# Performance work log

Hardware: AMD Instinct MI355X
Metric: run time of the kernel (lower is better)

Reference implementation:

```python
import jax, jax.numpy as jnp
import numpy as np

N = 50000      # nodes
E = 600000     # edges (avg degree 12)
D = 128        # input_dim == hidden_dim (required: same Linear reused across pool layers)
OUT = 64       # output_dim
NUM_POOL = 2   # num_pool_layers


def setup_inputs() -> dict:
    key = jax.random.key(0)
    ks = jax.random.split(key, 8)
    s = 1.0 / np.sqrt(D)  # fan-in style scaling keeps repeated scatter-adds stable
    x = jax.random.normal(ks[0], (N, D), dtype=jnp.float32)
    edge_index = jax.random.randint(ks[1], (2, E), 0, N, dtype=jnp.int64)
    W1 = jax.random.normal(ks[2], (D, D), dtype=jnp.float32) * s
    b1 = jnp.zeros((D,), dtype=jnp.float32)
    W2 = jax.random.normal(ks[3], (D, D), dtype=jnp.float32) * s
    b2 = jnp.zeros((D,), dtype=jnp.float32)
    Wout = jax.random.normal(ks[4], (D, OUT), dtype=jnp.float32) * s
    bout = jnp.zeros((OUT,), dtype=jnp.float32)
    return {"x": x, "edge_index": edge_index, "W1": W1, "b1": b1,
            "W2": W2, "b2": b2, "Wout": Wout, "bout": bout}


def _gauss_seidel_pool(x, W, b, src, dst, num_layers):
    # PyG MessagePassing(aggr='add'): out[i] = sum_{edges (j->i)} lin(x[j]).
    # Nodes with no incoming edges become zero (propagate replaces x entirely).
    for _ in range(num_layers):
        m = x @ W + b                      # [N, out] linear once per node (== lin(x_j) per edge)
        x = jax.ops.segment_sum(m[src], dst, num_segments=N)  # gather + scatter-add
    return x


def reference(x, edge_index, W1, b1, W2, b2, Wout, bout):
    src = edge_index[0]  # x_j source
    dst = edge_index[1]  # aggregation target i
    h = _gauss_seidel_pool(x, W1, b1, src, dst, NUM_POOL)
    h = jax.nn.relu(h)                     # dropout = identity (eval mode)
    h = _gauss_seidel_pool(h, W2, b2, src, dst, NUM_POOL)
    h = jax.nn.relu(h)
    return h @ Wout + bout                 # [N, OUT]
```

## Files before the change

### kernel.cpp

```cpp
#include <hip/hip_runtime.h>


static inline int ceil_div(int a, int b) { return (a + b - 1) / b; }

typedef __attribute__((ext_vector_type(8))) short bf16x8;
typedef __attribute__((ext_vector_type(4))) float f32x4;

__device__ inline unsigned short f2bf(float f) {
    unsigned u = __float_as_uint(f);
    return (unsigned short)((u + 0x7fffu + ((u >> 16) & 1u)) >> 16);
}


__device__ void wprep_dev(const float* __restrict__ W, unsigned short* __restrict__ hi,
                          int total, int C, int g0, int G) {
    for (int t = g0; t < total; t += G) {
        int j = t & 7;
        int lane = (t >> 3) & 63;
        int f = t >> 9;
        int c = f & 3, ct = f >> 2;
        int k = c * 32 + (lane >> 4) * 8 + j;
        int col = ct * 16 + (lane & 15);
        hi[t] = f2bf(W[(size_t)k * C + col]);
    }
}

__global__ __launch_bounds__(256) void prep_kernel(const float* __restrict__ W1,
                                                   const float* __restrict__ W2,
                                                   const float* __restrict__ Wout,
                                                   unsigned short* __restrict__ W1hi,
                                                   unsigned short* __restrict__ W2hi,
                                                   unsigned short* __restrict__ Wohi,
                                                   int* __restrict__ cursor,
                                                   unsigned* __restrict__ stat,
                                                   int N, int nChunks) {
    int g0 = blockIdx.x * 256 + threadIdx.x;
    int G = gridDim.x * 256;
    for (int i = g0; i < N; i += G) cursor[i] = 0;
    for (int i = g0; i < nChunks; i += G) stat[i] = 0;
    wprep_dev(W1, W1hi, 128 * 128, 128, g0, G);
    wprep_dev(W2, W2hi, 128 * 128, 128, g0, G);
    wprep_dev(Wout, Wohi, 128 * 64, 64, g0, G);
}


__global__ __launch_bounds__(256) void hist_kernel(const int* __restrict__ dst,
                                                   int* __restrict__ deg, int E) {
    int e = blockIdx.x * 256 + threadIdx.x;
    if (e < E) atomicAdd(&deg[dst[e]], 1);
}

__global__ __launch_bounds__(256) void scan_fuse_kernel(const int* __restrict__ deg,
                                                        int* __restrict__ rp,
                                                        int* __restrict__ cursor,
                                                        unsigned* __restrict__ stat,
                                                        int N) {
    __shared__ int s[256];
    int c = blockIdx.x, tid = threadIdx.x;
    int i = c * 256 + tid;
    int v = (i < N) ? deg[i] : 0;
    s[tid] = v;
    __syncthreads();
    for (int off = 1; off < 256; off <<= 1) {
        int t = (tid >= off) ? s[tid - off] : 0;
        __syncthreads();
        s[tid] += t;
        __syncthreads();
    }
    int loc = s[tid] - v;
    int tot = s[255];
    __syncthreads();
    if (tid == 0) atomicExch(&stat[c], (unsigned)tot | 0x80000000u);

    unsigned mine = 0;
    if (tid < c) {
        unsigned u;
        do { u = atomicAdd(&stat[tid], 0u); } while (!(u & 0x80000000u));
        mine = u & 0x7fffffffu;
    }
    s[tid] = (int)mine;
    __syncthreads();
    for (int off = 128; off >= 1; off >>= 1) {
        if (tid < off) s[tid] += s[tid + off];
        __syncthreads();
    }
    int prefix = s[0];
    if (i <= N) {
        int val = loc + prefix;
        rp[i] = val;
        if (i < N) cursor[i] = val;
    }
}

__global__ __launch_bounds__(256) void fill_kernel(const int* __restrict__ src,
                                                   const int* __restrict__ dst,
                                                   int* __restrict__ cursor,
                                                   unsigned short* __restrict__ es, int E) {
    int e = blockIdx.x * 256 + threadIdx.x;
    if (e < E) {
        int p = atomicAdd(&cursor[dst[e]], 1);
        es[p] = (unsigned short)src[e];
    }
}


__global__ __launch_bounds__(256) void gemm1_kernel(const float* __restrict__ X,
                                                    const uint4* __restrict__ Whi,
                                                    const float* __restrict__ Bias,
                                                    unsigned short* __restrict__ Y, int n) {
    int tid = threadIdx.x;
    int wave = tid >> 6, lane = tid & 63;
    int lm = lane & 15, lq = lane >> 4;
    int r0 = blockIdx.x * 64;

    bf16x8 afr[4][4];
#pragma unroll
    for (int rt = 0; rt < 4; ++rt) {
        int ar = r0 + rt * 16 + lm;
        if (ar > n - 1) ar = n - 1;
#pragma unroll
        for (int c = 0; c < 4; ++c) {
            int k = c * 32 + lq * 8;
            const float* ap = X + (size_t)ar * 128 + k;
            float4 f0 = ((const float4*)ap)[0];
            float4 f1 = ((const float4*)ap)[1];
            bf16x8 v;
            v[0] = (short)f2bf(f0.x); v[1] = (short)f2bf(f0.y);
            v[2] = (short)f2bf(f0.z); v[3] = (short)f2bf(f0.w);
            v[4] = (short)f2bf(f1.x); v[5] = (short)f2bf(f1.y);
            v[6] = (short)f2bf(f1.z); v[7] = (short)f2bf(f1.w);
            afr[rt][c] = v;
        }
    }

    f32x4 acc[4][2];
#pragma unroll
    for (int rt = 0; rt < 4; ++rt)
#pragma unroll
        for (int t = 0; t < 2; ++t)
            acc[rt][t] = (f32x4){0.f, 0.f, 0.f, 0.f};

#pragma unroll
    for (int c = 0; c < 4; ++c) {
#pragma unroll
        for (int t = 0; t < 2; ++t) {
            int ct = wave * 2 + t;
            uint4 uh = Whi[(ct * 4 + c) * 64 + lane];
            bf16x8 wh = *(const bf16x8*)&uh;
#pragma unroll
            for (int rt = 0; rt < 4; ++rt)
                acc[rt][t] = __builtin_amdgcn_mfma_f32_16x16x32_bf16(afr[rt][c], wh, acc[rt][t], 0, 0, 0);
        }
    }

#pragma unroll
    for (int t = 0; t < 2; ++t) {
        int col = (wave * 2 + t) * 16 + lm;
        float bias = Bias[col];
#pragma unroll
        for (int rt = 0; rt < 4; ++rt) {
#pragma unroll
            for (int r = 0; r < 4; ++r) {
                int row = r0 + rt * 16 + lq * 4 + r;
                if (row < n)
                    Y[(size_t)row * 128 + col] = f2bf(acc[rt][t][r] + bias);
            }
        }
    }
}


__device__ inline void acc_row8(float* a, uint4 v) {
    a[0] += __uint_as_float(v.x << 16);
    a[1] += __uint_as_float(v.x & 0xffff0000u);
    a[2] += __uint_as_float(v.y << 16);
    a[3] += __uint_as_float(v.y & 0xffff0000u);
    a[4] += __uint_as_float(v.z << 16);
    a[5] += __uint_as_float(v.z & 0xffff0000u);
    a[6] += __uint_as_float(v.w << 16);
    a[7] += __uint_as_float(v.w & 0xffff0000u);
}

template <int COLS, bool OUTF32>
__global__ __launch_bounds__(256) void fused_agg_gemm_kernel(const unsigned short* __restrict__ M,
                                                             const int* __restrict__ rp,
                                                             const unsigned short* __restrict__ es,
                                                             const uint4* __restrict__ Whi,
                                                             const float* __restrict__ Bias,
                                                             void* __restrict__ Yv,
                                                             int n, int do_relu) {
    constexpr int CT_W = COLS / 64;
    constexpr int SR = 136;
    __shared__ unsigned short Hl[64 * SR];
    __shared__ int rpl[65];
    __shared__ unsigned char perm[64];

    int tid = threadIdx.x;
    int r0 = blockIdx.x * 64;

    if (tid < 65) {
        int gi = r0 + tid;
        if (gi > n) gi = n;
        rpl[tid] = rp[gi];
    }
    __syncthreads();

    if (tid < 64) {
        int di = rpl[tid + 1] - rpl[tid];
        int rank = 0;
        for (int j = 0; j < 64; ++j) {
            int dj = rpl[j + 1] - rpl[j];
            rank += (dj > di) || (dj == di && j < tid);
        }
        perm[rank] = (unsigned char)tid;
    }
    __syncthreads();

    {
        int g = tid >> 4, ln = tid & 15;
#pragma unroll 1
        for (int q = 0; q < 4; ++q) {
            int nl = perm[q * 16 + g];
            int beg = rpl[nl], end = rpl[nl + 1];
            float acc[8] = {};
            int e = beg;
            for (; e + 8 <= end; e += 8) {
                int s0 = es[e],     s1 = es[e + 1], s2 = es[e + 2], s3 = es[e + 3];
                int s4 = es[e + 4], s5 = es[e + 5], s6 = es[e + 6], s7 = es[e + 7];
                uint4 v0 = ((const uint4*)(M + (size_t)s0 * 128))[ln];
                uint4 v1 = ((const uint4*)(M + (size_t)s1 * 128))[ln];
                uint4 v2 = ((const uint4*)(M + (size_t)s2 * 128))[ln];
                uint4 v3 = ((const uint4*)(M + (size_t)s3 * 128))[ln];
                uint4 v4 = ((const uint4*)(M + (size_t)s4 * 128))[ln];
                uint4 v5 = ((const uint4*)(M + (size_t)s5 * 128))[ln];
                uint4 v6 = ((const uint4*)(M + (size_t)s6 * 128))[ln];
                uint4 v7 = ((const uint4*)(M + (size_t)s7 * 128))[ln];
                acc_row8(acc, v0); acc_row8(acc, v1);
                acc_row8(acc, v2); acc_row8(acc, v3);
                acc_row8(acc, v4); acc_row8(acc, v5);
                acc_row8(acc, v6); acc_row8(acc, v7);
            }
            for (; e + 4 <= end; e += 4) {
                int s0 = es[e], s1 = es[e + 1], s2 = es[e + 2], s3 = es[e + 3];
                uint4 v0 = ((const uint4*)(M + (size_t)s0 * 128))[ln];
                uint4 v1 = ((const uint4*)(M + (size_t)s1 * 128))[ln];
                uint4 v2 = ((const uint4*)(M + (size_t)s2 * 128))[ln];
                uint4 v3 = ((const uint4*)(M + (size_t)s3 * 128))[ln];
                acc_row8(acc, v0); acc_row8(acc, v1);
                acc_row8(acc, v2); acc_row8(acc, v3);
            }
            for (; e < end; ++e) {
                uint4 v = ((const uint4*)(M + (size_t)es[e] * 128))[ln];
                acc_row8(acc, v);
            }
            if (do_relu) {
#pragma unroll
                for (int i = 0; i < 8; ++i) acc[i] = fmaxf(acc[i], 0.f);
            }
            uint4 o;
            o.x = (unsigned)f2bf(acc[0]) | ((unsigned)f2bf(acc[1]) << 16);
            o.y = (unsigned)f2bf(acc[2]) | ((unsigned)f2bf(acc[3]) << 16);
            o.z = (unsigned)f2bf(acc[4]) | ((unsigned)f2bf(acc[5]) << 16);
            o.w = (unsigned)f2bf(acc[6]) | ((unsigned)f2bf(acc[7]) << 16);
            *(uint4*)(&Hl[nl * SR + ln * 8]) = o;
        }
    }
    __syncthreads();

    int wave = tid >> 6, lane = tid & 63;
    int lm = lane & 15, lq = lane >> 4;

    f32x4 acc[4][CT_W];
#pragma unroll
    for (int rt = 0; rt < 4; ++rt)
#pragma unroll
        for (int t = 0; t < CT_W; ++t)
            acc[rt][t] = (f32x4){0.f, 0.f, 0.f, 0.f};

#pragma unroll
    for (int c = 0; c < 4; ++c) {
        bf16x8 afr[4];
#pragma unroll
        for (int rt = 0; rt < 4; ++rt)
            afr[rt] = *(const bf16x8*)(&Hl[(rt * 16 + lm) * SR + c * 32 + lq * 8]);
#pragma unroll
        for (int t = 0; t < CT_W; ++t) {
            int ct = wave * CT_W + t;
            uint4 uh = Whi[(ct * 4 + c) * 64 + lane];
            bf16x8 wh = *(const bf16x8*)&uh;
#pragma unroll
            for (int rt = 0; rt < 4; ++rt)
                acc[rt][t] = __builtin_amdgcn_mfma_f32_16x16x32_bf16(afr[rt], wh, acc[rt][t], 0, 0, 0);
        }
    }

#pragma unroll
    for (int t = 0; t < CT_W; ++t) {
        int col = (wave * CT_W + t) * 16 + lm;
        float bias = Bias[col];
#pragma unroll
        for (int rt = 0; rt < 4; ++rt) {
#pragma unroll
            for (int r = 0; r < 4; ++r) {
                int row = r0 + rt * 16 + lq * 4 + r;
                if (row < n) {
                    float v = acc[rt][t][r] + bias;
                    if (OUTF32)
                        ((float*)Yv)[(size_t)row * COLS + col] = v;
                    else
                        ((unsigned short*)Yv)[(size_t)row * COLS + col] = f2bf(v);
                }
            }
        }
    }
}


extern "C" void kernel_launch(void* const* d_in, const int* in_sizes, int n_in,
                              void* d_out, int out_size, void* d_ws, size_t ws_size,
                              hipStream_t stream) {
    const float* x    = (const float*)d_in[0];
    const int*   ei   = (const int*)d_in[1];
    const float* W1   = (const float*)d_in[2];
    const float* b1   = (const float*)d_in[3];
    const float* W2   = (const float*)d_in[4];
    const float* b2   = (const float*)d_in[5];
    const float* Wout = (const float*)d_in[6];
    const float* bout = (const float*)d_in[7];
    float*       out  = (float*)d_out;

    const int N = in_sizes[0] / 128;
    const int E = in_sizes[1] / 2;
    const int* src = ei;
    const int* dst = ei + E;

    char* ws = (char*)d_ws;
    auto take = [&](size_t bytes) {
        char* p = ws;
        ws += (bytes + 255) & ~(size_t)255;
        return p;
    };
    unsigned short* mA = (unsigned short*)take((size_t)N * 128 * 2);
    unsigned short* mB = (unsigned short*)take((size_t)N * 128 * 2);
    unsigned short* W1hi = (unsigned short*)take(128 * 128 * 2);
    unsigned short* W2hi = (unsigned short*)take(128 * 128 * 2);
    unsigned short* Wohi = (unsigned short*)take(128 * 64 * 2);
    int* rp      = (int*)take((size_t)(N + 1) * sizeof(int));
    int* cursor  = (int*)take((size_t)N * sizeof(int));
    unsigned short* es = (unsigned short*)take((size_t)E * sizeof(unsigned short));
    unsigned* stat = (unsigned*)take(4096);

    const int nChunks = ceil_div(N + 1, 256);
    const int tiles64 = ceil_div(N, 64);

    prep_kernel<<<256, 256, 0, stream>>>(W1, W2, Wout, W1hi, W2hi, Wohi,
                                         cursor, stat, N, nChunks);
    hist_kernel<<<ceil_div(E, 256), 256, 0, stream>>>(dst, cursor, E);
    scan_fuse_kernel<<<nChunks, 256, 0, stream>>>(cursor, rp, cursor, stat, N);
    fill_kernel<<<ceil_div(E, 256), 256, 0, stream>>>(src, dst, cursor, es, E);
    gemm1_kernel<<<tiles64, 256, 0, stream>>>(x, (const uint4*)W1hi, b1, mA, N);

    fused_agg_gemm_kernel<128, false><<<tiles64, 256, 0, stream>>>(
        mA, rp, es, (const uint4*)W1hi, b1, mB, N, 0);
    fused_agg_gemm_kernel<128, false><<<tiles64, 256, 0, stream>>>(
        mB, rp, es, (const uint4*)W2hi, b2, mA, N, 1);
    fused_agg_gemm_kernel<128, false><<<tiles64, 256, 0, stream>>>(
        mA, rp, es, (const uint4*)W2hi, b2, mB, N, 0);
    fused_agg_gemm_kernel<64, true><<<tiles64, 256, 0, stream>>>(
        mB, rp, es, (const uint4*)Wohi, bout, out, N, 1);
}
```

Before: 288.1 us.

## Reorder to aggregate-then-transform with degree-scaled bias and fused output GEMM

Uses linearity (sum of x_j W + b equals (sum x_j) W + deg*b) to aggregate raw features before each GEMM, removing the standalone first GEMM kernel in favour of a bf16 conversion of x in the prep kernel. The final GEMM with Wout is fused into the last aggregation kernel through shared memory, dropping one full-size kernel and its intermediate round trip. The gather loop now processes two destination nodes per thread group for more memory-level parallelism. It adds an extra bf16 copy of x and changes rounding order, so numerics differ slightly.

After: 337.3 us. 17.1% more time.

```diff
diff --git a/kernel.cpp b/kernel.cpp
--- a/kernel.cpp
+++ b/kernel.cpp
@@ -25,9 +25,11 @@
     }
 }
 
-__global__ __launch_bounds__(256) void prep_kernel(const float* __restrict__ W1,
+__global__ __launch_bounds__(256) void prep_kernel(const float* __restrict__ x,
+                                                   const float* __restrict__ W1,
                                                    const float* __restrict__ W2,
                                                    const float* __restrict__ Wout,
+                                                   unsigned short* __restrict__ xb,
                                                    unsigned short* __restrict__ W1hi,
                                                    unsigned short* __restrict__ W2hi,
                                                    unsigned short* __restrict__ Wohi,
@@ -38,6 +40,15 @@
     int G = gridDim.x * 256;
     for (int i = g0; i < N; i += G) cursor[i] = 0;
     for (int i = g0; i < nChunks; i += G) stat[i] = 0;
+
+    int nq = N * 32;
+    for (int i = g0; i < nq; i += G) {
+        float4 v = ((const float4*)x)[i];
+        ushort4 o;
+        o.x = f2bf(v.x); o.y = f2bf(v.y); o.z = f2bf(v.z); o.w = f2bf(v.w);
+        ((ushort4*)xb)[i] = o;
+    }
+
     wprep_dev(W1, W1hi, 128 * 128, 128, g0, G);
     wprep_dev(W2, W2hi, 128 * 128, 128, g0, G);
     wprep_dev(Wout, Wohi, 128 * 64, 64, g0, G);
@@ -104,72 +115,6 @@
 }
 
 
-__global__ __launch_bounds__(256) void gemm1_kernel(const float* __restrict__ X,
-                                                    const uint4* __restrict__ Whi,
-                                                    const float* __restrict__ Bias,
-                                                    unsigned short* __restrict__ Y, int n) {
-    int tid = threadIdx.x;
-    int wave = tid >> 6, lane = tid & 63;
-    int lm = lane & 15, lq = lane >> 4;
-    int r0 = blockIdx.x * 64;
-
-    bf16x8 afr[4][4];
-#pragma unroll
-    for (int rt = 0; rt < 4; ++rt) {
-        int ar = r0 + rt * 16 + lm;
-        if (ar > n - 1) ar = n - 1;
-#pragma unroll
-        for (int c = 0; c < 4; ++c) {
-            int k = c * 32 + lq * 8;
-            const float* ap = X + (size_t)ar * 128 + k;
-            float4 f0 = ((const float4*)ap)[0];
-            float4 f1 = ((const float4*)ap)[1];
-            bf16x8 v;
-            v[0] = (short)f2bf(f0.x); v[1] = (short)f2bf(f0.y);
-            v[2] = (short)f2bf(f0.z); v[3] = (short)f2bf(f0.w);
-            v[4] = (short)f2bf(f1.x); v[5] = (short)f2bf(f1.y);
-            v[6] = (short)f2bf(f1.z); v[7] = (short)f2bf(f1.w);
-            afr[rt][c] = v;
-        }
-    }
-
-    f32x4 acc[4][2];
-#pragma unroll
-    for (int rt = 0; rt < 4; ++rt)
-#pragma unroll
-        for (int t = 0; t < 2; ++t)
-            acc[rt][t] = (f32x4){0.f, 0.f, 0.f, 0.f};
-
-#pragma unroll
-    for (int c = 0; c < 4; ++c) {
-#pragma unroll
-        for (int t = 0; t < 2; ++t) {
-            int ct = wave * 2 + t;
-            uint4 uh = Whi[(ct * 4 + c) * 64 + lane];
-            bf16x8 wh = *(const bf16x8*)&uh;
-#pragma unroll
-            for (int rt = 0; rt < 4; ++rt)
-                acc[rt][t] = __builtin_amdgcn_mfma_f32_16x16x32_bf16(afr[rt][c], wh, acc[rt][t], 0, 0, 0);
-        }
-    }
-
-#pragma unroll
-    for (int t = 0; t < 2; ++t) {
-        int col = (wave * 2 + t) * 16 + lm;
-        float bias = Bias[col];
-#pragma unroll
-        for (int rt = 0; rt < 4; ++rt) {
-#pragma unroll
-            for (int r = 0; r < 4; ++r) {
-                int row = r0 + rt * 16 + lq * 4 + r;
-                if (row < n)
-                    Y[(size_t)row * 128 + col] = f2bf(acc[rt][t][r] + bias);
-            }
-        }
-    }
-}
-
-
 __device__ inline void acc_row8(float* a, uint4 v) {
     a[0] += __uint_as_float(v.x << 16);
     a[1] += __uint_as_float(v.x & 0xffff0000u);
@@ -181,15 +126,15 @@
     a[7] += __uint_as_float(v.w & 0xffff0000u);
 }
 
-template <int COLS, bool OUTF32>
-__global__ __launch_bounds__(256) void fused_agg_gemm_kernel(const unsigned short* __restrict__ M,
-                                                             const int* __restrict__ rp,
-                                                             const unsigned short* __restrict__ es,
-                                                             const uint4* __restrict__ Whi,
-                                                             const float* __restrict__ Bias,
-                                                             void* __restrict__ Yv,
-                                                             int n, int do_relu) {
-    constexpr int CT_W = COLS / 64;
+template <bool RELU, bool OUTCHAIN>
+__global__ __launch_bounds__(256) void fused_kernel(const unsigned short* __restrict__ M,
+                                                    const int* __restrict__ rp,
+                                                    const unsigned short* __restrict__ es,
+                                                    const uint4* __restrict__ Whi,
+                                                    const float* __restrict__ bvec,
+                                                    const uint4* __restrict__ Wof,
+                                                    const float* __restrict__ bout,
+                                                    void* __restrict__ Yv, int n) {
     constexpr int SR = 136;
     __shared__ unsigned short Hl[64 * SR];
     __shared__ int rpl[65];
@@ -219,50 +164,68 @@
     {
         int g = tid >> 4, ln = tid & 15;
 #pragma unroll 1
-        for (int q = 0; q < 4; ++q) {
-            int nl = perm[q * 16 + g];
-            int beg = rpl[nl], end = rpl[nl + 1];
-            float acc[8] = {};
-            int e = beg;
-            for (; e + 8 <= end; e += 8) {
-                int s0 = es[e],     s1 = es[e + 1], s2 = es[e + 2], s3 = es[e + 3];
-                int s4 = es[e + 4], s5 = es[e + 5], s6 = es[e + 6], s7 = es[e + 7];
-                uint4 v0 = ((const uint4*)(M + (size_t)s0 * 128))[ln];
-                uint4 v1 = ((const uint4*)(M + (size_t)s1 * 128))[ln];
-                uint4 v2 = ((const uint4*)(M + (size_t)s2 * 128))[ln];
-                uint4 v3 = ((const uint4*)(M + (size_t)s3 * 128))[ln];
-                uint4 v4 = ((const uint4*)(M + (size_t)s4 * 128))[ln];
-                uint4 v5 = ((const uint4*)(M + (size_t)s5 * 128))[ln];
-                uint4 v6 = ((const uint4*)(M + (size_t)s6 * 128))[ln];
-                uint4 v7 = ((const uint4*)(M + (size_t)s7 * 128))[ln];
-                acc_row8(acc, v0); acc_row8(acc, v1);
-                acc_row8(acc, v2); acc_row8(acc, v3);
-                acc_row8(acc, v4); acc_row8(acc, v5);
-                acc_row8(acc, v6); acc_row8(acc, v7);
-            }
-            for (; e + 4 <= end; e += 4) {
-                int s0 = es[e], s1 = es[e + 1], s2 = es[e + 2], s3 = es[e + 3];
-                uint4 v0 = ((const uint4*)(M + (size_t)s0 * 128))[ln];
-                uint4 v1 = ((const uint4*)(M + (size_t)s1 * 128))[ln];
-                uint4 v2 = ((const uint4*)(M + (size_t)s2 * 128))[ln];
-                uint4 v3 = ((const uint4*)(M + (size_t)s3 * 128))[ln];
-                acc_row8(acc, v0); acc_row8(acc, v1);
-                acc_row8(acc, v2); acc_row8(acc, v3);
-            }
-            for (; e < end; ++e) {
-                uint4 v = ((const uint4*)(M + (size_t)es[e] * 128))[ln];
-                acc_row8(acc, v);
-            }
-            if (do_relu) {
-#pragma unroll
-                for (int i = 0; i < 8; ++i) acc[i] = fmaxf(acc[i], 0.f);
-            }
-            uint4 o;
-            o.x = (unsigned)f2bf(acc[0]) | ((unsigned)f2bf(acc[1]) << 16);
-            o.y = (unsigned)f2bf(acc[2]) | ((unsigned)f2bf(acc[3]) << 16);
-            o.z = (unsigned)f2bf(acc[4]) | ((unsigned)f2bf(acc[5]) << 16);
-            o.w = (unsigned)f2bf(acc[6]) | ((unsigned)f2bf(acc[7]) << 16);
-            *(uint4*)(&Hl[nl * SR + ln * 8]) = o;
+        for (int q = 0; q < 2; ++q) {
+            int pr = (q * 16 + g) * 2;
+            int na = perm[pr], nb = perm[pr + 1];
+            int ea = rpl[na], enda = rpl[na + 1];
+            int eb = rpl[nb], endb = rpl[nb + 1];
+            float accA[8] = {}, accB[8] = {};
+
+            while (ea + 4 <= enda && eb + 4 <= endb) {
+                int a0 = es[ea], a1 = es[ea + 1], a2 = es[ea + 2], a3 = es[ea + 3];
+                int b0 = es[eb], b1 = es[eb + 1], b2 = es[eb + 2], b3 = es[eb + 3];
+                uint4 va0 = ((const uint4*)(M + (size_t)a0 * 128))[ln];
+                uint4 va1 = ((const uint4*)(M + (size_t)a1 * 128))[ln];
+                uint4 va2 = ((const uint4*)(M + (size_t)a2 * 128))[ln];
+                uint4 va3 = ((const uint4*)(M + (size_t)a3 * 128))[ln];
+                uint4 vb0 = ((const uint4*)(M + (size_t)b0 * 128))[ln];
+                uint4 vb1 = ((const uint4*)(M + (size_t)b1 * 128))[ln];
+                uint4 vb2 = ((const uint4*)(M + (size_t)b2 * 128))[ln];
+                uint4 vb3 = ((const uint4*)(M + (size_t)b3 * 128))[ln];
+                acc_row8(accA, va0); acc_row8(accA, va1);
+                acc_row8(accA, va2); acc_row8(accA, va3);
+                acc_row8(accB, vb0); acc_row8(accB, vb1);
+                acc_row8(accB, vb2); acc_row8(accB, vb3);
+                ea += 4; eb += 4;
+            }
+            for (; ea + 4 <= enda; ea += 4) {
+                int a0 = es[ea], a1 = es[ea + 1], a2 = es[ea + 2], a3 = es[ea + 3];
+                uint4 v0 = ((const uint4*)(M + (size_t)a0 * 128))[ln];
+                uint4 v1 = ((const uint4*)(M + (size_t)a1 * 128))[ln];
+                uint4 v2 = ((const uint4*)(M + (size_t)a2 * 128))[ln];
+                uint4 v3 = ((const uint4*)(M + (size_t)a3 * 128))[ln];
+                acc_row8(accA, v0); acc_row8(accA, v1);
+                acc_row8(accA, v2); acc_row8(accA, v3);
+            }
+            for (; ea < enda; ++ea) {
+                uint4 v = ((const uint4*)(M + (size_t)es[ea] * 128))[ln];
+                acc_row8(accA, v);
+            }
+            for (; eb + 4 <= endb; eb += 4) {
+                int b0 = es[eb], b1 = es[eb + 1], b2 = es[eb + 2], b3 = es[eb + 3];
+                uint4 v0 = ((const uint4*)(M + (size_t)b0 * 128))[ln];
+                uint4 v1 = ((const uint4*)(M + (size_t)b1 * 128))[ln];
+                uint4 v2 = ((const uint4*)(M + (size_t)b2 * 128))[ln];
+                uint4 v3 = ((const uint4*)(M + (size_t)b3 * 128))[ln];
+                acc_row8(accB, v0); acc_row8(accB, v1);
+                acc_row8(accB, v2); acc_row8(accB, v3);
+            }
+            for (; eb < endb; ++eb) {
+                uint4 v = ((const uint4*)(M + (size_t)es[eb] * 128))[ln];
+                acc_row8(accB, v);
+            }
+
+            uint4 oA, oB;
+            oA.x = (unsigned)f2bf(accA[0]) | ((unsigned)f2bf(accA[1]) << 16);
+            oA.y = (unsigned)f2bf(accA[2]) | ((unsigned)f2bf(accA[3]) << 16);
+            oA.z = (unsigned)f2bf(accA[4]) | ((unsigned)f2bf(accA[5]) << 16);
+            oA.w = (unsigned)f2bf(accA[6]) | ((unsigned)f2bf(accA[7]) << 16);
+            oB.x = (unsigned)f2bf(accB[0]) | ((unsigned)f2bf(accB[1]) << 16);
+            oB.y = (unsigned)f2bf(accB[2]) | ((unsigned)f2bf(accB[3]) << 16);
+            oB.z = (unsigned)f2bf(accB[4]) | ((unsigned)f2bf(accB[5]) << 16);
+            oB.w = (unsigned)f2bf(accB[6]) | ((unsigned)f2bf(accB[7]) << 16);
+            *(uint4*)(&Hl[na * SR + ln * 8]) = oA;
+            *(uint4*)(&Hl[nb * SR + ln * 8]) = oB;
         }
     }
     __syncthreads();
@@ -270,11 +233,11 @@
     int wave = tid >> 6, lane = tid & 63;
     int lm = lane & 15, lq = lane >> 4;
 
-    f32x4 acc[4][CT_W];
+    f32x4 acc[4][2];
 #pragma unroll
     for (int rt = 0; rt < 4; ++rt)
 #pragma unroll
-        for (int t = 0; t < CT_W; ++t)
+        for (int t = 0; t < 2; ++t)
             acc[rt][t] = (f32x4){0.f, 0.f, 0.f, 0.f};
 
 #pragma unroll
@@ -284,8 +247,8 @@
         for (int rt = 0; rt < 4; ++rt)
             afr[rt] = *(const bf16x8*)(&Hl[(rt * 16 + lm) * SR + c * 32 + lq * 8]);
 #pragma unroll
-        for (int t = 0; t < CT_W; ++t) {
-            int ct = wave * CT_W + t;
+        for (int t = 0; t < 2; ++t) {
+            int ct = wave * 2 + t;
             uint4 uh = Whi[(ct * 4 + c) * 64 + lane];
             bf16x8 wh = *(const bf16x8*)&uh;
 #pragma unroll
@@ -294,22 +257,72 @@
         }
     }
 
-#pragma unroll
-    for (int t = 0; t < CT_W; ++t) {
-        int col = (wave * CT_W + t) * 16 + lm;
-        float bias = Bias[col];
+    if (!OUTCHAIN) {
+#pragma unroll
+        for (int t = 0; t < 2; ++t) {
+            int col = (wave * 2 + t) * 16 + lm;
+            float bv = bvec[col];
+#pragma unroll
+            for (int rt = 0; rt < 4; ++rt) {
+#pragma unroll
+                for (int r = 0; r < 4; ++r) {
+                    int rowl = rt * 16 + lq * 4 + r;
+                    int row = r0 + rowl;
+                    if (row < n) {
+                        float deg = (float)(rpl[rowl + 1] - rpl[rowl]);
+                        float v = acc[rt][t][r] + deg * bv;
+                        if (RELU) v = fmaxf(v, 0.f);
+                        ((unsigned short*)Yv)[(size_t)row * 128 + col] = f2bf(v);
+                    }
+                }
+            }
+        }
+    } else {
+        __syncthreads();
+#pragma unroll
+        for (int t = 0; t < 2; ++t) {
+            int col = (wave * 2 + t) * 16 + lm;
+            float bv = bvec[col];
+#pragma unroll
+            for (int rt = 0; rt < 4; ++rt) {
+#pragma unroll
+                for (int r = 0; r < 4; ++r) {
+                    int rowl = rt * 16 + lq * 4 + r;
+                    float deg = (float)(rpl[rowl + 1] - rpl[rowl]);
+                    float v = acc[rt][t][r] + deg * bv;
+                    v = fmaxf(v, 0.f);
+                    Hl[rowl * SR + col] = f2bf(v);
+                }
+            }
+        }
+        __syncthreads();
+
+        f32x4 acc2[4];
+#pragma unroll
+        for (int rt = 0; rt < 4; ++rt) acc2[rt] = (f32x4){0.f, 0.f, 0.f, 0.f};
+
+#pragma unroll
+        for (int c = 0; c < 4; ++c) {
+            bf16x8 afr[4];
+#pragma unroll
+            for (int rt = 0; rt < 4; ++rt)
+                afr[rt] = *(const bf16x8*)(&Hl[(rt * 16 + lm) * SR + c * 32 + lq * 8]);
+            uint4 uw = Wof[(wave * 4 + c) * 64 + lane];
+            bf16x8 wf = *(const bf16x8*)&uw;
+#pragma unroll
+            for (int rt = 0; rt < 4; ++rt)
+                acc2[rt] = __builtin_amdgcn_mfma_f32_16x16x32_bf16(afr[rt], wf, acc2[rt], 0, 0, 0);
+        }
+
+        int col = wave * 16 + lm;
+        float bo = bout[col];
 #pragma unroll
         for (int rt = 0; rt < 4; ++rt) {
 #pragma unroll
             for (int r = 0; r < 4; ++r) {
                 int row = r0 + rt * 16 + lq * 4 + r;
-                if (row < n) {
-                    float v = acc[rt][t][r] + bias;
-                    if (OUTF32)
-                        ((float*)Yv)[(size_t)row * COLS + col] = v;
-                    else
-                        ((unsigned short*)Yv)[(size_t)row * COLS + col] = f2bf(v);
-                }
+                if (row < n)
+                    ((float*)Yv)[(size_t)row * 64 + col] = acc2[rt][r] + bo;
             }
         }
     }
@@ -340,6 +353,7 @@
         ws += (bytes + 255) & ~(size_t)255;
         return p;
     };
+    unsigned short* xb = (unsigned short*)take((size_t)N * 128 * 2);
     unsigned short* mA = (unsigned short*)take((size_t)N * 128 * 2);
     unsigned short* mB = (unsigned short*)take((size_t)N * 128 * 2);
     unsigned short* W1hi = (unsigned short*)take(128 * 128 * 2);
@@ -353,19 +367,18 @@
     const int nChunks = ceil_div(N + 1, 256);
     const int tiles64 = ceil_div(N, 64);
 
-    prep_kernel<<<256, 256, 0, stream>>>(W1, W2, Wout, W1hi, W2hi, Wohi,
+    prep_kernel<<<256, 256, 0, stream>>>(x, W1, W2, Wout, xb, W1hi, W2hi, Wohi,
                                          cursor, stat, N, nChunks);
     hist_kernel<<<ceil_div(E, 256), 256, 0, stream>>>(dst, cursor, E);
     scan_fuse_kernel<<<nChunks, 256, 0, stream>>>(cursor, rp, cursor, stat, N);
     fill_kernel<<<ceil_div(E, 256), 256, 0, stream>>>(src, dst, cursor, es, E);
-    gemm1_kernel<<<tiles64, 256, 0, stream>>>(x, (const uint4*)W1hi, b1, mA, N);
-
-    fused_agg_gemm_kernel<128, false><<<tiles64, 256, 0, stream>>>(
-        mA, rp, es, (const uint4*)W1hi, b1, mB, N, 0);
-    fused_agg_gemm_kernel<128, false><<<tiles64, 256, 0, stream>>>(
-        mB, rp, es, (const uint4*)W2hi, b2, mA, N, 1);
-    fused_agg_gemm_kernel<128, false><<<tiles64, 256, 0, stream>>>(
-        mA, rp, es, (const uint4*)W2hi, b2, mB, N, 0);
-    fused_agg_gemm_kernel<64, true><<<tiles64, 256, 0, stream>>>(
-        mB, rp, es, (const uint4*)Wohi, bout, out, N, 1);
-}
+
+    fused_kernel<false, false><<<tiles64, 256, 0, stream>>>(
+        xb, rp, es, (const uint4*)W1hi, b1, nullptr, nullptr, mA, N);
+    fused_kernel<true, false><<<tiles64, 256, 0, stream>>>(
+        mA, rp, es, (const uint4*)W1hi, b1, nullptr, nullptr, mB, N);
+    fused_kernel<false, false><<<tiles64, 256, 0, stream>>>(
+        mB, rp, es, (const uint4*)W2hi, b2, nullptr, nullptr, mA, N);
+    fused_kernel<true, true><<<tiles64, 256, 0, stream>>>(
+        mA, rp, es, (const uint4*)W2hi, b2, (const uint4*)Wohi, bout, out, N);
+}
```
